# Kernel optimization log

Measured on AMD Instinct MI355X. Metric: run time of the kernel, lower is better.

Reference implementation:

```python
import jax, jax.numpy as jnp
import numpy as np

N_NODES = 50000
N_EDGES = 800000
IN_CH = 64
HID = 64
E_FEAT = 16


def _gcn_conv(x, W, b, row, col, n_nodes):
    """PyG-style GCNConv: add self loops, symmetric normalization,
    aggregate messages from source (row) at target (col)."""
    h = x @ W  # [N, H]
    loops = jnp.arange(n_nodes, dtype=row.dtype)
    r = jnp.concatenate([row, loops])
    c = jnp.concatenate([col, loops])
    ones = jnp.ones(r.shape[0], dtype=h.dtype)
    deg = jax.ops.segment_sum(ones, c, num_segments=n_nodes)  # in-degree incl. self loop
    dinv = jnp.where(deg > 0, deg ** -0.5, 0.0)
    norm = dinv[r] * dinv[c]  # [E+N]
    msg = h[r] * norm[:, None]  # gather + scale
    out = jax.ops.segment_sum(msg, c, num_segments=n_nodes)  # scatter-add at targets
    return out + b


def setup_inputs() -> dict:
    key = jax.random.key(0)
    ks = jax.random.split(key, 10)
    x = jax.random.normal(ks[0], (N_NODES, IN_CH), dtype=jnp.float32)
    eIndex = jax.random.randint(ks[1], (2, N_EDGES), 0, N_NODES, dtype=jnp.int32)
    eAttributes = jax.random.normal(ks[2], (N_EDGES, E_FEAT), dtype=jnp.float32)
    s1 = 1.0 / np.sqrt(IN_CH)
    s2 = 1.0 / np.sqrt(HID)
    sm = 1.0 / np.sqrt(2 * HID + E_FEAT)
    W1 = jax.random.uniform(ks[3], (IN_CH, HID), jnp.float32, -s1, s1)
    b1 = jnp.zeros((HID,), jnp.float32)
    W2 = jax.random.uniform(ks[4], (HID, HID), jnp.float32, -s2, s2)
    b2 = jnp.zeros((HID,), jnp.float32)
    mW1 = jax.random.uniform(ks[5], (2 * HID + E_FEAT, HID), jnp.float32, -sm, sm)
    mb1 = jax.random.uniform(ks[6], (HID,), jnp.float32, -sm, sm)
    mW2 = jax.random.uniform(ks[7], (HID, 1), jnp.float32, -s2, s2)
    mb2 = jax.random.uniform(ks[8], (1,), jnp.float32, -s2, s2)
    return {"x": x, "eIndex": eIndex, "eAttributes": eAttributes,
            "W1": W1, "b1": b1, "W2": W2, "b2": b2,
            "mW1": mW1, "mb1": mb1, "mW2": mW2, "mb2": mb2}


def reference(x, eIndex, eAttributes, W1, b1, W2, b2, mW1, mb1, mW2, mb2):
    row, col = eIndex[0], eIndex[1]
    n = x.shape[0]
    h = _gcn_conv(x, W1, b1, row, col, n)
    h = jax.nn.relu(h)
    h = _gcn_conv(h, W2, b2, row, col, n)
    # edge gather-concat-MLP
    ef = jnp.concatenate([h[row], h[col], eAttributes], axis=1)  # [E, 2H+F]
    out = jax.nn.relu(ef @ mW1 + mb1) @ mW2 + mb2  # [E, 1]
    return out
```

## Files before the change

### kernel.cpp

```cpp
#include <hip/hip_runtime.h>
#include <hip/hip_bf16.h>
#include <hip/hip_fp16.h>

#define N_NODES 50000
#define N_EDGES 800000
#define E_FEAT 16
#define BUCKET 64
#define NSL 200
#define SLW 250
#define P1B 200
#define EPB 4000
#define QCAP 64
#define GEMM1_BLOCKS 512

typedef _Float16 half4_t __attribute__((ext_vector_type(4)));
typedef _Float16 half8_t __attribute__((ext_vector_type(8)));
typedef float f32x4 __attribute__((ext_vector_type(4)));

template <int NF, bool DUAL, bool SCALE>
__device__ __forceinline__ void gemm_body(const float* __restrict__ X,
                                          const float* __restrict__ WA,
                                          const float* __restrict__ WB,
                                          const float* __restrict__ scale,
                                          const float* __restrict__ bias,
                                          __half* __restrict__ YA, __half* __restrict__ YB,
                                          int N, int wid, int nw, int lane) {
    int grp = lane >> 4, sub = lane & 15;

    half4_t wf[NF][4];
#pragma unroll
    for (int fc = 0; fc < NF; ++fc) {
        const float* Wsrc = (DUAL && fc >= NF / 2) ? WB : WA;
        int f = 16 * (DUAL ? (fc % (NF / 2)) : fc) + sub;
#pragma unroll
        for (int kc = 0; kc < 4; ++kc)
#pragma unroll
            for (int i = 0; i < 4; ++i)
                wf[fc][kc][i] = (_Float16)Wsrc[(16 * kc + 4 * grp + i) * 64 + f];
    }
    float bval[NF];
#pragma unroll
    for (int fc = 0; fc < NF; ++fc)
        bval[fc] = (DUAL && fc < NF / 2) ? bias[16 * fc + sub] : 0.0f;

    int ntiles = N >> 4;
    for (int t = wid; t < ntiles; t += nw) {
        int r0 = t << 4;
        half4_t a[4];
#pragma unroll
        for (int kc = 0; kc < 4; ++kc) {
            float4 xv = *(const float4*)(X + (size_t)(r0 + sub) * 64 + 16 * kc + 4 * grp);
            a[kc][0] = (_Float16)xv.x; a[kc][1] = (_Float16)xv.y;
            a[kc][2] = (_Float16)xv.z; a[kc][3] = (_Float16)xv.w;
        }
        f32x4 acc[NF];
#pragma unroll
        for (int fc = 0; fc < NF; ++fc) {
            float b = bval[fc];
            acc[fc][0] = b; acc[fc][1] = b; acc[fc][2] = b; acc[fc][3] = b;
        }
#pragma unroll
        for (int fc = 0; fc < NF; ++fc)
#pragma unroll
            for (int kc = 0; kc < 4; ++kc)
                acc[fc] = __builtin_amdgcn_mfma_f32_16x16x16f16(a[kc], wf[fc][kc], acc[fc], 0, 0, 0);

        float scv[4] = {1.f, 1.f, 1.f, 1.f};
        if (SCALE) {
            float4 sc = *(const float4*)(scale + r0 + 4 * grp);
            scv[0] = sc.x; scv[1] = sc.y; scv[2] = sc.z; scv[3] = sc.w;
        }
#pragma unroll
        for (int fc = 0; fc < NF; ++fc) {
            __half* Y = (DUAL && fc >= NF / 2) ? YB : YA;
            int f = 16 * (DUAL ? (fc % (NF / 2)) : fc) + sub;
#pragma unroll
            for (int reg = 0; reg < 4; ++reg) {
                float v = acc[fc][reg];
                if (SCALE) v *= scv[reg];
                Y[(size_t)(r0 + 4 * grp + reg) * 64 + f] = __float2half_rn(v);
            }
        }
    }
}

template <int NF, bool DUAL, bool SCALE>
__global__ void gemm_mfma_kernel(const float* __restrict__ X,
                                 const float* __restrict__ WA, const float* __restrict__ WB,
                                 const float* __restrict__ scale, const float* __restrict__ bias,
                                 __half* __restrict__ YA, __half* __restrict__ YB, int N) {
    int lane = threadIdx.x & 63;
    int wid = (blockIdx.x * blockDim.x + threadIdx.x) >> 6;
    int nw = (gridDim.x * blockDim.x) >> 6;
    gemm_body<NF, DUAL, SCALE>(X, WA, WB, scale, bias, YA, YB, N, wid, nw, lane);
}

__global__ void partition_gemm_kernel(const int* __restrict__ row, const int* __restrict__ col,
                                      unsigned int* __restrict__ queue, int* __restrict__ lens,
                                      const float* __restrict__ X, const float* __restrict__ W,
                                      __half* __restrict__ Y, int N) {
    if (blockIdx.x < P1B) {
        __shared__ int cur[NSL];
        for (int i = threadIdx.x; i < NSL; i += blockDim.x) cur[i] = 0;
        __syncthreads();
        int b = blockIdx.x;
        int base = b * EPB;
        for (int e = base + (int)threadIdx.x * 4; e < base + EPB; e += blockDim.x * 4) {
            int4 c4 = *(const int4*)(col + e);
            int4 r4 = *(const int4*)(row + e);
            int s, p;
            s = c4.x / SLW; p = atomicAdd(&cur[s], 1);
            if (p < QCAP) queue[(size_t)(b * NSL + s) * QCAP + p] = ((unsigned)c4.x << 16) | (unsigned)r4.x;
            s = c4.y / SLW; p = atomicAdd(&cur[s], 1);
            if (p < QCAP) queue[(size_t)(b * NSL + s) * QCAP + p] = ((unsigned)c4.y << 16) | (unsigned)r4.y;
            s = c4.z / SLW; p = atomicAdd(&cur[s], 1);
            if (p < QCAP) queue[(size_t)(b * NSL + s) * QCAP + p] = ((unsigned)c4.z << 16) | (unsigned)r4.z;
            s = c4.w / SLW; p = atomicAdd(&cur[s], 1);
            if (p < QCAP) queue[(size_t)(b * NSL + s) * QCAP + p] = ((unsigned)c4.w << 16) | (unsigned)r4.w;
        }
        __syncthreads();
        for (int i = threadIdx.x; i < NSL; i += blockDim.x)
            lens[b * NSL + i] = min(cur[i], QCAP);
    } else {
        int lane = threadIdx.x & 63;
        int wid = ((blockIdx.x - P1B) * 256 + (int)threadIdx.x) >> 6;
        int nw = (GEMM1_BLOCKS * 256) >> 6;
        gemm_body<4, false, false>(X, W, W, nullptr, nullptr, Y, Y, N, wid, nw, lane);
    }
}

__global__ void scatter3_kernel(const unsigned int* __restrict__ queue,
                                const int* __restrict__ lens,
                                int* __restrict__ cnt, float* __restrict__ dinv,
                                unsigned short* __restrict__ srcIdx) {
    __shared__ int lcnt[SLW];
    int s = blockIdx.x;
    for (int i = threadIdx.x; i < SLW; i += blockDim.x) lcnt[i] = 0;
    __syncthreads();
    int cbase = s * SLW;
    if (threadIdx.x < P1B) {
        int b = threadIdx.x;
        int len = lens[b * NSL + s];
        const unsigned int* q = queue + (size_t)(b * NSL + s) * QCAP;
        unsigned int nxt = (len > 0) ? q[0] : 0u;
        for (int i = 0; i < len; ++i) {
            unsigned int pr = nxt;
            if (i + 1 < len) nxt = q[i + 1];
            int c = (int)(pr >> 16);
            int r = (int)(pr & 0xffffu);
            int p = atomicAdd(&lcnt[c - cbase], 1);
            if (p < BUCKET) srcIdx[(c << 6) + p] = (unsigned short)r;
        }
    }
    __syncthreads();
    for (int i = threadIdx.x; i < SLW; i += blockDim.x) {
        int d = lcnt[i];
        cnt[cbase + i] = d;
        dinv[cbase + i] = rsqrtf((float)d + 1.0f);
    }
}

template <bool RELU, bool SRCSCALED>
__global__ void agg_bucket_kernel(const float2* __restrict__ hs4,
                                  const int* __restrict__ cnt,
                                  const float* __restrict__ dinv,
                                  const unsigned short* __restrict__ srcIdx,
                                  const float* __restrict__ b,
                                  float4* __restrict__ out, int N) {
    int lane = threadIdx.x & 63;
    int n = blockIdx.x * (blockDim.x >> 6) + (threadIdx.x >> 6);
    if (n >= N) return;
    int g = lane >> 4;
    int sub = lane & 15;
    int o = n << 6;
    int d = min(cnt[n], BUCKET);
    float dinvn = dinv[n];
    float4 acc = make_float4(0.f, 0.f, 0.f, 0.f);
    if (g == 0) {
        float2 raw = hs4[(size_t)n * 16 + sub];
        float2 a01 = __half22float2(*(const __half2*)&raw.x);
        float2 a23 = __half22float2(*(const __half2*)&raw.y);
        float w = SRCSCALED ? 1.0f : dinvn;
        acc.x = a01.x * w; acc.y = a01.y * w;
        acc.z = a23.x * w; acc.w = a23.y * w;
    }
    int j = g;
    for (; j + 12 < d; j += 16) {
        int s0 = srcIdx[o + j],     s1 = srcIdx[o + j + 4];
        int s2 = srcIdx[o + j + 8], s3 = srcIdx[o + j + 12];
        float2 v0 = hs4[(size_t)s0 * 16 + sub];
        float2 v1 = hs4[(size_t)s1 * 16 + sub];
        float2 v2 = hs4[(size_t)s2 * 16 + sub];
        float2 v3 = hs4[(size_t)s3 * 16 + sub];
        float w0 = 1.f, w1 = 1.f, w2 = 1.f, w3 = 1.f;
        if (!SRCSCALED) {
            w0 = rsqrtf((float)cnt[s0] + 1.f); w1 = rsqrtf((float)cnt[s1] + 1.f);
            w2 = rsqrtf((float)cnt[s2] + 1.f); w3 = rsqrtf((float)cnt[s3] + 1.f);
        }
        float2 a01 = __half22float2(*(const __half2*)&v0.x);
        float2 a23 = __half22float2(*(const __half2*)&v0.y);
        float2 b01 = __half22float2(*(const __half2*)&v1.x);
        float2 b23 = __half22float2(*(const __half2*)&v1.y);
        float2 c01 = __half22float2(*(const __half2*)&v2.x);
        float2 c23 = __half22float2(*(const __half2*)&v2.y);
        float2 d01 = __half22float2(*(const __half2*)&v3.x);
        float2 d23 = __half22float2(*(const __half2*)&v3.y);
        acc.x = fmaf(a01.x, w0, fmaf(b01.x, w1, fmaf(c01.x, w2, fmaf(d01.x, w3, acc.x))));
        acc.y = fmaf(a01.y, w0, fmaf(b01.y, w1, fmaf(c01.y, w2, fmaf(d01.y, w3, acc.y))));
        acc.z = fmaf(a23.x, w0, fmaf(b23.x, w1, fmaf(c23.x, w2, fmaf(d23.x, w3, acc.z))));
        acc.w = fmaf(a23.y, w0, fmaf(b23.y, w1, fmaf(c23.y, w2, fmaf(d23.y, w3, acc.w))));
    }
    for (; j + 4 < d; j += 8) {
        int s0 = srcIdx[o + j];
        int s1 = srcIdx[o + j + 4];
        float2 v0 = hs4[(size_t)s0 * 16 + sub];
        float2 v1 = hs4[(size_t)s1 * 16 + sub];
        float w0 = 1.f, w1 = 1.f;
        if (!SRCSCALED) {
            w0 = rsqrtf((float)cnt[s0] + 1.f); w1 = rsqrtf((float)cnt[s1] + 1.f);
        }
        float2 a01 = __half22float2(*(const __half2*)&v0.x);
        float2 a23 = __half22float2(*(const __half2*)&v0.y);
        float2 b01 = __half22float2(*(const __half2*)&v1.x);
        float2 b23 = __half22float2(*(const __half2*)&v1.y);
        acc.x = fmaf(a01.x, w0, fmaf(b01.x, w1, acc.x));
        acc.y = fmaf(a01.y, w0, fmaf(b01.y, w1, acc.y));
        acc.z = fmaf(a23.x, w0, fmaf(b23.x, w1, acc.z));
        acc.w = fmaf(a23.y, w0, fmaf(b23.y, w1, acc.w));
    }
    for (; j < d; j += 4) {
        int s0 = srcIdx[o + j];
        float2 v = hs4[(size_t)s0 * 16 + sub];
        float w0 = SRCSCALED ? 1.f : rsqrtf((float)cnt[s0] + 1.f);
        float2 a01 = __half22float2(*(const __half2*)&v.x);
        float2 a23 = __half22float2(*(const __half2*)&v.y);
        acc.x = fmaf(a01.x, w0, acc.x); acc.y = fmaf(a01.y, w0, acc.y);
        acc.z = fmaf(a23.x, w0, acc.z); acc.w = fmaf(a23.y, w0, acc.w);
    }
    acc.x += __shfl_xor(acc.x, 16); acc.y += __shfl_xor(acc.y, 16);
    acc.z += __shfl_xor(acc.z, 16); acc.w += __shfl_xor(acc.w, 16);
    acc.x += __shfl_xor(acc.x, 32); acc.y += __shfl_xor(acc.y, 32);
    acc.z += __shfl_xor(acc.z, 32); acc.w += __shfl_xor(acc.w, 32);
    if (g == 0) {
        float4 bb = ((const float4*)b)[sub];
        float4 v;
        v.x = fmaf(dinvn, acc.x, bb.x); v.y = fmaf(dinvn, acc.y, bb.y);
        v.z = fmaf(dinvn, acc.z, bb.z); v.w = fmaf(dinvn, acc.w, bb.w);
        if (RELU) {
            v.x = fmaxf(v.x, 0.f); v.y = fmaxf(v.y, 0.f);
            v.z = fmaxf(v.z, 0.f); v.w = fmaxf(v.w, 0.f);
        }
        out[(size_t)n * 16 + sub] = v;
    }
}

__global__ void edge_mlp6_kernel(const __half* __restrict__ P16, const __half* __restrict__ Q16,
                                 const int* __restrict__ row, const int* __restrict__ col,
                                 const float* __restrict__ eAtt,
                                 const float* __restrict__ mW1,
                                 const float* __restrict__ mW2, const float* __restrict__ mb2,
                                 float* __restrict__ out, int E) {
    int lane = threadIdx.x & 63;
    int grp = lane >> 4;
    int sub = lane & 15;

    half4_t aC0, aC1, aC2, aC3;
#pragma unroll
    for (int i = 0; i < 4; ++i) {
        const float* crow = mW1 + (size_t)(128 + 4 * grp + i) * 64 + 4 * sub;
        aC0[i] = (_Float16)crow[0];
        aC1[i] = (_Float16)crow[1];
        aC2[i] = (_Float16)crow[2];
        aC3[i] = (_Float16)crow[3];
    }
    float4 w20 = ((const float4*)mW2)[4 * grp + 0];
    float4 w21 = ((const float4*)mW2)[4 * grp + 1];
    float4 w22 = ((const float4*)mW2)[4 * grp + 2];
    float4 w23 = ((const float4*)mW2)[4 * grp + 3];
    float b2v = mb2[0];

    int wid = (blockIdx.x * blockDim.x + threadIdx.x) >> 6;
    int nw = (gridDim.x * blockDim.x) >> 6;
    const int ntiles = E >> 4;

    int rA = 0, cA = 0, rB = 0, cB = 0;
    if (wid < ntiles) {
        rA = __builtin_nontemporal_load(row + (wid << 4) + sub);
        cA = __builtin_nontemporal_load(col + (wid << 4) + sub);
    }
    if (wid + nw < ntiles) {
        rB = __builtin_nontemporal_load(row + ((wid + nw) << 4) + sub);
        cB = __builtin_nontemporal_load(col + ((wid + nw) << 4) + sub);
    }

    int t = wid;
    for (; t + nw < ntiles; t += 2 * nw) {
        int eA0 = t << 4, eB0 = (t + nw) << 4;

        f32x4 efA = __builtin_nontemporal_load((const f32x4*)(eAtt + (size_t)eA0 * 16) + (size_t)sub * 4 + grp);
        f32x4 efB = __builtin_nontemporal_load((const f32x4*)(eAtt + (size_t)eB0 * 16) + (size_t)sub * 4 + grp);
        const half8_t* prA = (const half8_t*)(P16 + (size_t)rA * 64 + grp * 16);
        const half8_t* qrA = (const half8_t*)(Q16 + (size_t)cA * 64 + grp * 16);
        const half8_t* prB = (const half8_t*)(P16 + (size_t)rB * 64 + grp * 16);
        const half8_t* qrB = (const half8_t*)(Q16 + (size_t)cB * 64 + grp * 16);
        half8_t phA0 = prA[0], phA1 = prA[1], qhA0 = qrA[0], qhA1 = qrA[1];
        half8_t phB0 = prB[0], phB1 = prB[1], qhB0 = qrB[0], qhB1 = qrB[1];

        int tn1 = t + 2 * nw, tn2 = t + 3 * nw;
        int rA2 = 0, cA2 = 0, rB2 = 0, cB2 = 0;
        if (tn1 < ntiles) {
            rA2 = __builtin_nontemporal_load(row + (tn1 << 4) + sub);
            cA2 = __builtin_nontemporal_load(col + (tn1 << 4) + sub);
        }
        if (tn2 < ntiles) {
            rB2 = __builtin_nontemporal_load(row + (tn2 << 4) + sub);
            cB2 = __builtin_nontemporal_load(col + (tn2 << 4) + sub);
        }

        half4_t bfA;
        bfA[0] = (_Float16)efA[0]; bfA[1] = (_Float16)efA[1];
        bfA[2] = (_Float16)efA[2]; bfA[3] = (_Float16)efA[3];
        f32x4 cin0 = {(float)phA0[0] + (float)qhA0[0], (float)phA0[4] + (float)qhA0[4],
                      (float)phA1[0] + (float)qhA1[0], (float)phA1[4] + (float)qhA1[4]};
        f32x4 cin1 = {(float)phA0[1] + (float)qhA0[1], (float)phA0[5] + (float)qhA0[5],
                      (float)phA1[1] + (float)qhA1[1], (float)phA1[5] + (float)qhA1[5]};
        f32x4 cin2 = {(float)phA0[2] + (float)qhA0[2], (float)phA0[6] + (float)qhA0[6],
                      (float)phA1[2] + (float)qhA1[2], (float)phA1[6] + (float)qhA1[6]};
        f32x4 cin3 = {(float)phA0[3] + (float)qhA0[3], (float)phA0[7] + (float)qhA0[7],
                      (float)phA1[3] + (float)qhA1[3], (float)phA1[7] + (float)qhA1[7]};
        f32x4 d0 = __builtin_amdgcn_mfma_f32_16x16x16f16(aC0, bfA, cin0, 0, 0, 0);
        f32x4 d1 = __builtin_amdgcn_mfma_f32_16x16x16f16(aC1, bfA, cin1, 0, 0, 0);
        f32x4 d2 = __builtin_amdgcn_mfma_f32_16x16x16f16(aC2, bfA, cin2, 0, 0, 0);
        f32x4 d3 = __builtin_amdgcn_mfma_f32_16x16x16f16(aC3, bfA, cin3, 0, 0, 0);
        float taccA = fmaxf(d0[0], 0.f) * w20.x + fmaxf(d0[1], 0.f) * w21.x
                    + fmaxf(d0[2], 0.f) * w22.x + fmaxf(d0[3], 0.f) * w23.x;
        taccA += fmaxf(d1[0], 0.f) * w20.y + fmaxf(d1[1], 0.f) * w21.y
               + fmaxf(d1[2], 0.f) * w22.y + fmaxf(d1[3], 0.f) * w23.y;
        taccA += fmaxf(d2[0], 0.f) * w20.z + fmaxf(d2[1], 0.f) * w21.z
               + fmaxf(d2[2], 0.f) * w22.z + fmaxf(d2[3], 0.f) * w23.z;
        taccA += fmaxf(d3[0], 0.f) * w20.w + fmaxf(d3[1], 0.f) * w21.w
               + fmaxf(d3[2], 0.f) * w22.w + fmaxf(d3[3], 0.f) * w23.w;

        half4_t bfB;
        bfB[0] = (_Float16)efB[0]; bfB[1] = (_Float16)efB[1];
        bfB[2] = (_Float16)efB[2]; bfB[3] = (_Float16)efB[3];
        cin0 = f32x4{(float)phB0[0] + (float)qhB0[0], (float)phB0[4] + (float)qhB0[4],
                     (float)phB1[0] + (float)qhB1[0], (float)phB1[4] + (float)qhB1[4]};
        cin1 = f32x4{(float)phB0[1] + (float)qhB0[1], (float)phB0[5] + (float)qhB0[5],
                     (float)phB1[1] + (float)qhB1[1], (float)phB1[5] + (float)qhB1[5]};
        cin2 = f32x4{(float)phB0[2] + (float)qhB0[2], (float)phB0[6] + (float)qhB0[6],
                     (float)phB1[2] + (float)qhB1[2], (float)phB1[6] + (float)qhB1[6]};
        cin3 = f32x4{(float)phB0[3] + (float)qhB0[3], (float)phB0[7] + (float)qhB0[7],
                     (float)phB1[3] + (float)qhB1[3], (float)phB1[7] + (float)qhB1[7]};
        d0 = __builtin_amdgcn_mfma_f32_16x16x16f16(aC0, bfB, cin0, 0, 0, 0);
        d1 = __builtin_amdgcn_mfma_f32_16x16x16f16(aC1, bfB, cin1, 0, 0, 0);
        d2 = __builtin_amdgcn_mfma_f32_16x16x16f16(aC2, bfB, cin2, 0, 0, 0);
        d3 = __builtin_amdgcn_mfma_f32_16x16x16f16(aC3, bfB, cin3, 0, 0, 0);
        float taccB = fmaxf(d0[0], 0.f) * w20.x + fmaxf(d0[1], 0.f) * w21.x
                    + fmaxf(d0[2], 0.f) * w22.x + fmaxf(d0[3], 0.f) * w23.x;
        taccB += fmaxf(d1[0], 0.f) * w20.y + fmaxf(d1[1], 0.f) * w21.y
               + fmaxf(d1[2], 0.f) * w22.y + fmaxf(d1[3], 0.f) * w23.y;
        taccB += fmaxf(d2[0], 0.f) * w20.z + fmaxf(d2[1], 0.f) * w21.z
               + fmaxf(d2[2], 0.f) * w22.z + fmaxf(d2[3], 0.f) * w23.z;
        taccB += fmaxf(d3[0], 0.f) * w20.w + fmaxf(d3[1], 0.f) * w21.w
               + fmaxf(d3[2], 0.f) * w22.w + fmaxf(d3[3], 0.f) * w23.w;

        taccA += __shfl_xor(taccA, 16); taccB += __shfl_xor(taccB, 16);
        taccA += __shfl_xor(taccA, 32); taccB += __shfl_xor(taccB, 32);
        if (grp == 0) {
            __builtin_nontemporal_store(taccA + b2v, out + eA0 + sub);
            __builtin_nontemporal_store(taccB + b2v, out + eB0 + sub);
        }

        rA = rA2; cA = cA2; rB = rB2; cB = cB2;
    }
    if (t < ntiles) {
        int e0 = t << 4;
        f32x4 ef = __builtin_nontemporal_load((const f32x4*)(eAtt + (size_t)e0 * 16) + (size_t)sub * 4 + grp);
        half4_t bf;
        bf[0] = (_Float16)ef[0]; bf[1] = (_Float16)ef[1];
        bf[2] = (_Float16)ef[2]; bf[3] = (_Float16)ef[3];
        const half8_t* pr = (const half8_t*)(P16 + (size_t)rA * 64 + grp * 16);
        const half8_t* qr = (const half8_t*)(Q16 + (size_t)cA * 64 + grp * 16);
        half8_t ph0 = pr[0], ph1 = pr[1], qh0 = qr[0], qh1 = qr[1];
        f32x4 cin0 = {(float)ph0[0] + (float)qh0[0], (float)ph0[4] + (float)qh0[4],
                      (float)ph1[0] + (float)qh1[0], (float)ph1[4] + (float)qh1[4]};
        f32x4 cin1 = {(float)ph0[1] + (float)qh0[1], (float)ph0[5] + (float)qh0[5],
                      (float)ph1[1] + (float)qh1[1], (float)ph1[5] + (float)qh1[5]};
        f32x4 cin2 = {(float)ph0[2] + (float)qh0[2], (float)ph0[6] + (float)qh0[6],
                      (float)ph1[2] + (float)qh1[2], (float)ph1[6] + (float)qh1[6]};
        f32x4 cin3 = {(float)ph0[3] + (float)qh0[3], (float)ph0[7] + (float)qh0[7],
                      (float)ph1[3] + (float)qh1[3], (float)ph1[7] + (float)qh1[7]};
        f32x4 d0 = __builtin_amdgcn_mfma_f32_16x16x16f16(aC0, bf, cin0, 0, 0, 0);
        f32x4 d1 = __builtin_amdgcn_mfma_f32_16x16x16f16(aC1, bf, cin1, 0, 0, 0);
        f32x4 d2 = __builtin_amdgcn_mfma_f32_16x16x16f16(aC2, bf, cin2, 0, 0, 0);
        f32x4 d3 = __builtin_amdgcn_mfma_f32_16x16x16f16(aC3, bf, cin3, 0, 0, 0);
        float tacc = fmaxf(d0[0], 0.f) * w20.x + fmaxf(d0[1], 0.f) * w21.x
                   + fmaxf(d0[2], 0.f) * w22.x + fmaxf(d0[3], 0.f) * w23.x;
        tacc += fmaxf(d1[0], 0.f) * w20.y + fmaxf(d1[1], 0.f) * w21.y
              + fmaxf(d1[2], 0.f) * w22.y + fmaxf(d1[3], 0.f) * w23.y;
        tacc += fmaxf(d2[0], 0.f) * w20.z + fmaxf(d2[1], 0.f) * w21.z
              + fmaxf(d2[2], 0.f) * w22.z + fmaxf(d2[3], 0.f) * w23.z;
        tacc += fmaxf(d3[0], 0.f) * w20.w + fmaxf(d3[1], 0.f) * w21.w
              + fmaxf(d3[2], 0.f) * w22.w + fmaxf(d3[3], 0.f) * w23.w;
        tacc += __shfl_xor(tacc, 16);
        tacc += __shfl_xor(tacc, 32);
        if (grp == 0) __builtin_nontemporal_store(tacc + b2v, out + e0 + sub);
    }
}

extern "C" void kernel_launch(void* const* d_in, const int* in_sizes, int n_in,
                              void* d_out, int out_size, void* d_ws, size_t ws_size,
                              hipStream_t stream) {
    const float* x    = (const float*)d_in[0];
    const int*   eIdx = (const int*)d_in[1];
    const float* eAtt = (const float*)d_in[2];
    const float* W1   = (const float*)d_in[3];
    const float* b1   = (const float*)d_in[4];
    const float* W2   = (const float*)d_in[5];
    const float* b2   = (const float*)d_in[6];
    const float* mW1  = (const float*)d_in[7];
    const float* mb1  = (const float*)d_in[8];
    const float* mW2  = (const float*)d_in[9];
    const float* mb2  = (const float*)d_in[10];
    float* out = (float*)d_out;

    const int N = N_NODES;
    const int E = N_EDGES;
    const int* row = eIdx;
    const int* col = eIdx + E;

    int*            cnt    = (int*)d_ws;
    float*          dinv   = (float*)(cnt + ((N + 63) & ~63));
    int*            lens   = (int*)(dinv + ((N + 63) & ~63));
    unsigned int*   queue  = (unsigned int*)(lens + P1B * NSL);
    unsigned short* srcIdx = (unsigned short*)(queue + (size_t)P1B * NSL * QCAP);
    __half*         h16    = (__half*)(srcIdx + (size_t)N * BUCKET);
    float*          bufB   = (float*)(h16 + (size_t)2 * N * 64);
    __half*         P16    = h16;
    __half*         Q16    = h16 + (size_t)N * 64;

    const int aggBlocks = (N + 3) / 4;

    partition_gemm_kernel<<<P1B + GEMM1_BLOCKS, 256, 0, stream>>>(
        row, col, queue, lens, x, W1, h16, N);
    scatter3_kernel<<<NSL, 256, 0, stream>>>(queue, lens, cnt, dinv, srcIdx);

    agg_bucket_kernel<true, false><<<aggBlocks, 256, 0, stream>>>(
        (const float2*)h16, cnt, dinv, srcIdx, b1, (float4*)bufB, N);

    gemm_mfma_kernel<4, false, true><<<800, 256, 0, stream>>>(
        bufB, W2, W2, dinv, nullptr, h16, h16, N);
    agg_bucket_kernel<false, true><<<aggBlocks, 256, 0, stream>>>(
        (const float2*)h16, cnt, dinv, srcIdx, b2, (float4*)bufB, N);

    gemm_mfma_kernel<8, true, false><<<800, 256, 0, stream>>>(
        bufB, mW1, mW1 + 64 * 64, nullptr, mb1, P16, Q16, N);

    edge_mlp6_kernel<<<3125, 256, 0, stream>>>(
        P16, Q16, row, col, eAtt, mW1, mW2, mb2, out, E);
}
```

Before: 139.4 us.

## Fuse neighbor aggregation with following dense GEMM via LDS staging

Each aggregation kernel now processes 16 nodes per block, writes the aggregated rows into shared memory, then runs the 64x64 MFMA GEMM on that tile directly. This replaces the separate aggregation and GEMM launches for both GCN layers and drops the fp32 intermediate buffer round trip through global memory. A separate half buffer (hs2) avoids reading and writing h16 in the same kernel. The edge MLP grid is also reduced from 3125 to 2048 blocks. The tradeoff is fewer nodes in flight per block during the gather phase, plus a block-wide barrier and redundant weight loads per block.

```diff
diff --git a/kernel.cpp b/kernel.cpp
--- a/kernel.cpp
+++ b/kernel.cpp
@@ -12,36 +12,29 @@
 #define EPB 4000
 #define QCAP 64
 #define GEMM1_BLOCKS 512
+#define HSTRIDE 72
 
 typedef _Float16 half4_t __attribute__((ext_vector_type(4)));
 typedef _Float16 half8_t __attribute__((ext_vector_type(8)));
 typedef float f32x4 __attribute__((ext_vector_type(4)));
 
-template <int NF, bool DUAL, bool SCALE>
+template <int NF>
 __device__ __forceinline__ void gemm_body(const float* __restrict__ X,
-                                          const float* __restrict__ WA,
-                                          const float* __restrict__ WB,
-                                          const float* __restrict__ scale,
-                                          const float* __restrict__ bias,
-                                          __half* __restrict__ YA, __half* __restrict__ YB,
+                                          const float* __restrict__ W,
+                                          __half* __restrict__ Y,
                                           int N, int wid, int nw, int lane) {
     int grp = lane >> 4, sub = lane & 15;
 
     half4_t wf[NF][4];
 #pragma unroll
     for (int fc = 0; fc < NF; ++fc) {
-        const float* Wsrc = (DUAL && fc >= NF / 2) ? WB : WA;
-        int f = 16 * (DUAL ? (fc % (NF / 2)) : fc) + sub;
+        int f = 16 * fc + sub;
 #pragma unroll
         for (int kc = 0; kc < 4; ++kc)
 #pragma unroll
             for (int i = 0; i < 4; ++i)
-                wf[fc][kc][i] = (_Float16)Wsrc[(16 * kc + 4 * grp + i) * 64 + f];
-    }
-    float bval[NF];
-#pragma unroll
-    for (int fc = 0; fc < NF; ++fc)
-        bval[fc] = (DUAL && fc < NF / 2) ? bias[16 * fc + sub] : 0.0f;
+                wf[fc][kc][i] = (_Float16)W[(16 * kc + 4 * grp + i) * 64 + f];
+    }
 
     int ntiles = N >> 4;
     for (int t = wid; t < ntiles; t += nw) {
@@ -55,44 +48,20 @@
         }
         f32x4 acc[NF];
 #pragma unroll
-        for (int fc = 0; fc < NF; ++fc) {
-            float b = bval[fc];
-            acc[fc][0] = b; acc[fc][1] = b; acc[fc][2] = b; acc[fc][3] = b;
-        }
+        for (int fc = 0; fc < NF; ++fc) { acc[fc][0] = 0; acc[fc][1] = 0; acc[fc][2] = 0; acc[fc][3] = 0; }
 #pragma unroll
         for (int fc = 0; fc < NF; ++fc)
 #pragma unroll
             for (int kc = 0; kc < 4; ++kc)
                 acc[fc] = __builtin_amdgcn_mfma_f32_16x16x16f16(a[kc], wf[fc][kc], acc[fc], 0, 0, 0);
-
-        float scv[4] = {1.f, 1.f, 1.f, 1.f};
-        if (SCALE) {
-            float4 sc = *(const float4*)(scale + r0 + 4 * grp);
-            scv[0] = sc.x; scv[1] = sc.y; scv[2] = sc.z; scv[3] = sc.w;
-        }
 #pragma unroll
         for (int fc = 0; fc < NF; ++fc) {
-            __half* Y = (DUAL && fc >= NF / 2) ? YB : YA;
-            int f = 16 * (DUAL ? (fc % (NF / 2)) : fc) + sub;
-#pragma unroll
-            for (int reg = 0; reg < 4; ++reg) {
-                float v = acc[fc][reg];
-                if (SCALE) v *= scv[reg];
-                Y[(size_t)(r0 + 4 * grp + reg) * 64 + f] = __float2half_rn(v);
-            }
-        }
-    }
-}
-
-template <int NF, bool DUAL, bool SCALE>
-__global__ void gemm_mfma_kernel(const float* __restrict__ X,
-                                 const float* __restrict__ WA, const float* __restrict__ WB,
-                                 const float* __restrict__ scale, const float* __restrict__ bias,
-                                 __half* __restrict__ YA, __half* __restrict__ YB, int N) {
-    int lane = threadIdx.x & 63;
-    int wid = (blockIdx.x * blockDim.x + threadIdx.x) >> 6;
-    int nw = (gridDim.x * blockDim.x) >> 6;
-    gemm_body<NF, DUAL, SCALE>(X, WA, WB, scale, bias, YA, YB, N, wid, nw, lane);
+            int f = 16 * fc + sub;
+#pragma unroll
+            for (int reg = 0; reg < 4; ++reg)
+                Y[(size_t)(r0 + 4 * grp + reg) * 64 + f] = __float2half_rn(acc[fc][reg]);
+        }
+    }
 }
 
 __global__ void partition_gemm_kernel(const int* __restrict__ row, const int* __restrict__ col,
@@ -125,7 +94,7 @@
         int lane = threadIdx.x & 63;
         int wid = ((blockIdx.x - P1B) * 256 + (int)threadIdx.x) >> 6;
         int nw = (GEMM1_BLOCKS * 256) >> 6;
-        gemm_body<4, false, false>(X, W, W, nullptr, nullptr, Y, Y, N, wid, nw, lane);
+        gemm_body<4>(X, W, Y, N, wid, nw, lane);
     }
 }
 
@@ -160,97 +129,146 @@
     }
 }
 
-template <bool RELU, bool SRCSCALED>
-__global__ void agg_bucket_kernel(const float2* __restrict__ hs4,
-                                  const int* __restrict__ cnt,
-                                  const float* __restrict__ dinv,
-                                  const unsigned short* __restrict__ srcIdx,
-                                  const float* __restrict__ b,
-                                  float4* __restrict__ out, int N) {
+template <bool RELU_H, bool SRCSCALED, bool DUALOUT, bool SCALEOUT>
+__global__ void fused_agg_gemm_kernel(const float2* __restrict__ hs4,
+                                      const int* __restrict__ cnt,
+                                      const float* __restrict__ dinv,
+                                      const unsigned short* __restrict__ srcIdx,
+                                      const float* __restrict__ bagg,
+                                      const float* __restrict__ WA, const float* __restrict__ WB,
+                                      const float* __restrict__ biasP,
+                                      __half* __restrict__ YA, __half* __restrict__ YB, int N) {
+    __shared__ float hlds[16 * HSTRIDE];
     int lane = threadIdx.x & 63;
-    int n = blockIdx.x * (blockDim.x >> 6) + (threadIdx.x >> 6);
-    if (n >= N) return;
+    int w = threadIdx.x >> 6;
     int g = lane >> 4;
     int sub = lane & 15;
-    int o = n << 6;
-    int d = min(cnt[n], BUCKET);
-    float dinvn = dinv[n];
-    float4 acc = make_float4(0.f, 0.f, 0.f, 0.f);
-    if (g == 0) {
-        float2 raw = hs4[(size_t)n * 16 + sub];
-        float2 a01 = __half22float2(*(const __half2*)&raw.x);
-        float2 a23 = __half22float2(*(const __half2*)&raw.y);
-        float w = SRCSCALED ? 1.0f : dinvn;
-        acc.x = a01.x * w; acc.y = a01.y * w;
-        acc.z = a23.x * w; acc.w = a23.y * w;
-    }
-    int j = g;
-    for (; j + 12 < d; j += 16) {
-        int s0 = srcIdx[o + j],     s1 = srcIdx[o + j + 4];
-        int s2 = srcIdx[o + j + 8], s3 = srcIdx[o + j + 12];
-        float2 v0 = hs4[(size_t)s0 * 16 + sub];
-        float2 v1 = hs4[(size_t)s1 * 16 + sub];
-        float2 v2 = hs4[(size_t)s2 * 16 + sub];
-        float2 v3 = hs4[(size_t)s3 * 16 + sub];
-        float w0 = 1.f, w1 = 1.f, w2 = 1.f, w3 = 1.f;
-        if (!SRCSCALED) {
-            w0 = rsqrtf((float)cnt[s0] + 1.f); w1 = rsqrtf((float)cnt[s1] + 1.f);
-            w2 = rsqrtf((float)cnt[s2] + 1.f); w3 = rsqrtf((float)cnt[s3] + 1.f);
-        }
-        float2 a01 = __half22float2(*(const __half2*)&v0.x);
-        float2 a23 = __half22float2(*(const __half2*)&v0.y);
-        float2 b01 = __half22float2(*(const __half2*)&v1.x);
-        float2 b23 = __half22float2(*(const __half2*)&v1.y);
-        float2 c01 = __half22float2(*(const __half2*)&v2.x);
-        float2 c23 = __half22float2(*(const __half2*)&v2.y);
-        float2 d01 = __half22float2(*(const __half2*)&v3.x);
-        float2 d23 = __half22float2(*(const __half2*)&v3.y);
-        acc.x = fmaf(a01.x, w0, fmaf(b01.x, w1, fmaf(c01.x, w2, fmaf(d01.x, w3, acc.x))));
-        acc.y = fmaf(a01.y, w0, fmaf(b01.y, w1, fmaf(c01.y, w2, fmaf(d01.y, w3, acc.y))));
-        acc.z = fmaf(a23.x, w0, fmaf(b23.x, w1, fmaf(c23.x, w2, fmaf(d23.x, w3, acc.z))));
-        acc.w = fmaf(a23.y, w0, fmaf(b23.y, w1, fmaf(c23.y, w2, fmaf(d23.y, w3, acc.w))));
-    }
-    for (; j + 4 < d; j += 8) {
-        int s0 = srcIdx[o + j];
-        int s1 = srcIdx[o + j + 4];
-        float2 v0 = hs4[(size_t)s0 * 16 + sub];
-        float2 v1 = hs4[(size_t)s1 * 16 + sub];
-        float w0 = 1.f, w1 = 1.f;
-        if (!SRCSCALED) {
-            w0 = rsqrtf((float)cnt[s0] + 1.f); w1 = rsqrtf((float)cnt[s1] + 1.f);
-        }
-        float2 a01 = __half22float2(*(const __half2*)&v0.x);
-        float2 a23 = __half22float2(*(const __half2*)&v0.y);
-        float2 b01 = __half22float2(*(const __half2*)&v1.x);
-        float2 b23 = __half22float2(*(const __half2*)&v1.y);
-        acc.x = fmaf(a01.x, w0, fmaf(b01.x, w1, acc.x));
-        acc.y = fmaf(a01.y, w0, fmaf(b01.y, w1, acc.y));
-        acc.z = fmaf(a23.x, w0, fmaf(b23.x, w1, acc.z));
-        acc.w = fmaf(a23.y, w0, fmaf(b23.y, w1, acc.w));
-    }
-    for (; j < d; j += 4) {
-        int s0 = srcIdx[o + j];
-        float2 v = hs4[(size_t)s0 * 16 + sub];
-        float w0 = SRCSCALED ? 1.f : rsqrtf((float)cnt[s0] + 1.f);
-        float2 a01 = __half22float2(*(const __half2*)&v.x);
-        float2 a23 = __half22float2(*(const __half2*)&v.y);
-        acc.x = fmaf(a01.x, w0, acc.x); acc.y = fmaf(a01.y, w0, acc.y);
-        acc.z = fmaf(a23.x, w0, acc.z); acc.w = fmaf(a23.y, w0, acc.w);
-    }
-    acc.x += __shfl_xor(acc.x, 16); acc.y += __shfl_xor(acc.y, 16);
-    acc.z += __shfl_xor(acc.z, 16); acc.w += __shfl_xor(acc.w, 16);
-    acc.x += __shfl_xor(acc.x, 32); acc.y += __shfl_xor(acc.y, 32);
-    acc.z += __shfl_xor(acc.z, 32); acc.w += __shfl_xor(acc.w, 32);
-    if (g == 0) {
-        float4 bb = ((const float4*)b)[sub];
-        float4 v;
-        v.x = fmaf(dinvn, acc.x, bb.x); v.y = fmaf(dinvn, acc.y, bb.y);
-        v.z = fmaf(dinvn, acc.z, bb.z); v.w = fmaf(dinvn, acc.w, bb.w);
-        if (RELU) {
-            v.x = fmaxf(v.x, 0.f); v.y = fmaxf(v.y, 0.f);
-            v.z = fmaxf(v.z, 0.f); v.w = fmaxf(v.w, 0.f);
-        }
-        out[(size_t)n * 16 + sub] = v;
+    int grp = g;
+    int n0 = blockIdx.x << 4;
+
+    for (int k = 0; k < 4; ++k) {
+        int n = n0 + 4 * w + k;
+        int o = n << 6;
+        int d = min(cnt[n], BUCKET);
+        float dinvn = dinv[n];
+        float4 acc = make_float4(0.f, 0.f, 0.f, 0.f);
+        if (g == 0) {
+            float2 raw = hs4[(size_t)n * 16 + sub];
+            float2 a01 = __half22float2(*(const __half2*)&raw.x);
+            float2 a23 = __half22float2(*(const __half2*)&raw.y);
+            float ws = SRCSCALED ? 1.0f : dinvn;
+            acc.x = a01.x * ws; acc.y = a01.y * ws;
+            acc.z = a23.x * ws; acc.w = a23.y * ws;
+        }
+        int j = g;
+        for (; j + 12 < d; j += 16) {
+            int s0 = srcIdx[o + j],     s1 = srcIdx[o + j + 4];
+            int s2 = srcIdx[o + j + 8], s3 = srcIdx[o + j + 12];
+            float2 v0 = hs4[(size_t)s0 * 16 + sub];
+            float2 v1 = hs4[(size_t)s1 * 16 + sub];
+            float2 v2 = hs4[(size_t)s2 * 16 + sub];
+            float2 v3 = hs4[(size_t)s3 * 16 + sub];
+            float w0 = 1.f, w1 = 1.f, w2 = 1.f, w3 = 1.f;
+            if (!SRCSCALED) {
+                w0 = rsqrtf((float)cnt[s0] + 1.f); w1 = rsqrtf((float)cnt[s1] + 1.f);
+                w2 = rsqrtf((float)cnt[s2] + 1.f); w3 = rsqrtf((float)cnt[s3] + 1.f);
+            }
+            float2 a01 = __half22float2(*(const __half2*)&v0.x);
+            float2 a23 = __half22float2(*(const __half2*)&v0.y);
+            float2 b01 = __half22float2(*(const __half2*)&v1.x);
+            float2 b23 = __half22float2(*(const __half2*)&v1.y);
+            float2 c01 = __half22float2(*(const __half2*)&v2.x);
+            float2 c23 = __half22float2(*(const __half2*)&v2.y);
+            float2 d01 = __half22float2(*(const __half2*)&v3.x);
+            float2 d23 = __half22float2(*(const __half2*)&v3.y);
+            acc.x = fmaf(a01.x, w0, fmaf(b01.x, w1, fmaf(c01.x, w2, fmaf(d01.x, w3, acc.x))));
+            acc.y = fmaf(a01.y, w0, fmaf(b01.y, w1, fmaf(c01.y, w2, fmaf(d01.y, w3, acc.y))));
+            acc.z = fmaf(a23.x, w0, fmaf(b23.x, w1, fmaf(c23.x, w2, fmaf(d23.x, w3, acc.z))));
+            acc.w = fmaf(a23.y, w0, fmaf(b23.y, w1, fmaf(c23.y, w2, fmaf(d23.y, w3, acc.w))));
+        }
+        for (; j + 4 < d; j += 8) {
+            int s0 = srcIdx[o + j];
+            int s1 = srcIdx[o + j + 4];
+            float2 v0 = hs4[(size_t)s0 * 16 + sub];
+            float2 v1 = hs4[(size_t)s1 * 16 + sub];
+            float w0 = 1.f, w1 = 1.f;
+            if (!SRCSCALED) {
+                w0 = rsqrtf((float)cnt[s0] + 1.f); w1 = rsqrtf((float)cnt[s1] + 1.f);
+            }
+            float2 a01 = __half22float2(*(const __half2*)&v0.x);
+            float2 a23 = __half22float2(*(const __half2*)&v0.y);
+            float2 b01 = __half22float2(*(const __half2*)&v1.x);
+            float2 b23 = __half22float2(*(const __half2*)&v1.y);
+            acc.x = fmaf(a01.x, w0, fmaf(b01.x, w1, acc.x));
+            acc.y = fmaf(a01.y, w0, fmaf(b01.y, w1, acc.y));
+            acc.z = fmaf(a23.x, w0, fmaf(b23.x, w1, acc.z));
+            acc.w = fmaf(a23.y, w0, fmaf(b23.y, w1, acc.w));
+        }
+        for (; j < d; j += 4) {
+            int s0 = srcIdx[o + j];
+            float2 v = hs4[(size_t)s0 * 16 + sub];
+            float w0 = SRCSCALED ? 1.f : rsqrtf((float)cnt[s0] + 1.f);
+            float2 a01 = __half22float2(*(const __half2*)&v.x);
+            float2 a23 = __half22float2(*(const __half2*)&v.y);
+            acc.x = fmaf(a01.x, w0, acc.x); acc.y = fmaf(a01.y, w0, acc.y);
+            acc.z = fmaf(a23.x, w0, acc.z); acc.w = fmaf(a23.y, w0, acc.w);
+        }
+        acc.x += __shfl_xor(acc.x, 16); acc.y += __shfl_xor(acc.y, 16);
+        acc.z += __shfl_xor(acc.z, 16); acc.w += __shfl_xor(acc.w, 16);
+        acc.x += __shfl_xor(acc.x, 32); acc.y += __shfl_xor(acc.y, 32);
+        acc.z += __shfl_xor(acc.z, 32); acc.w += __shfl_xor(acc.w, 32);
+        if (g == 0) {
+            float4 bb = ((const float4*)bagg)[sub];
+            float4 v;
+            v.x = fmaf(dinvn, acc.x, bb.x); v.y = fmaf(dinvn, acc.y, bb.y);
+            v.z = fmaf(dinvn, acc.z, bb.z); v.w = fmaf(dinvn, acc.w, bb.w);
+            if (RELU_H) {
+                v.x = fmaxf(v.x, 0.f); v.y = fmaxf(v.y, 0.f);
+                v.z = fmaxf(v.z, 0.f); v.w = fmaxf(v.w, 0.f);
+            }
+            *(float4*)&hlds[(4 * w + k) * HSTRIDE + 4 * sub] = v;
+        }
+    }
+    __syncthreads();
+
+    int f = 16 * w + sub;
+    half4_t wfa[4], wfb[4];
+#pragma unroll
+    for (int kc = 0; kc < 4; ++kc)
+#pragma unroll
+        for (int i = 0; i < 4; ++i) {
+            wfa[kc][i] = (_Float16)WA[(16 * kc + 4 * grp + i) * 64 + f];
+            if (DUALOUT) wfb[kc][i] = (_Float16)WB[(16 * kc + 4 * grp + i) * 64 + f];
+        }
+
+    half4_t a[4];
+#pragma unroll
+    for (int kc = 0; kc < 4; ++kc) {
+        float4 xv = *(const float4*)&hlds[sub * HSTRIDE + 16 * kc + 4 * grp];
+        a[kc][0] = (_Float16)xv.x; a[kc][1] = (_Float16)xv.y;
+        a[kc][2] = (_Float16)xv.z; a[kc][3] = (_Float16)xv.w;
+    }
+
+    float bp = DUALOUT ? biasP[f] : 0.0f;
+    f32x4 accA = {bp, bp, bp, bp};
+    f32x4 accB = {0.f, 0.f, 0.f, 0.f};
+#pragma unroll
+    for (int kc = 0; kc < 4; ++kc) {
+        accA = __builtin_amdgcn_mfma_f32_16x16x16f16(a[kc], wfa[kc], accA, 0, 0, 0);
+        if (DUALOUT) accB = __builtin_amdgcn_mfma_f32_16x16x16f16(a[kc], wfb[kc], accB, 0, 0, 0);
+    }
+
+    float scv[4] = {1.f, 1.f, 1.f, 1.f};
+    if (SCALEOUT) {
+        float4 sc = *(const float4*)(dinv + n0 + 4 * grp);
+        scv[0] = sc.x; scv[1] = sc.y; scv[2] = sc.z; scv[3] = sc.w;
+    }
+#pragma unroll
+    for (int reg = 0; reg < 4; ++reg) {
+        float vA = accA[reg];
+        if (SCALEOUT) vA *= scv[reg];
+        YA[(size_t)(n0 + 4 * grp + reg) * 64 + f] = __float2half_rn(vA);
+        if (DUALOUT) YB[(size_t)(n0 + 4 * grp + reg) * 64 + f] = __float2half_rn(accB[reg]);
     }
 }
 
@@ -436,27 +454,24 @@
     unsigned int*   queue  = (unsigned int*)(lens + P1B * NSL);
     unsigned short* srcIdx = (unsigned short*)(queue + (size_t)P1B * NSL * QCAP);
     __half*         h16    = (__half*)(srcIdx + (size_t)N * BUCKET);
-    float*          bufB   = (float*)(h16 + (size_t)2 * N * 64);
     __half*         P16    = h16;
     __half*         Q16    = h16 + (size_t)N * 64;
-
-    const int aggBlocks = (N + 3) / 4;
+    __half*         hs2    = (__half*)(h16 + (size_t)2 * N * 64);
+
+    const int fusedBlocks = N / 16;
 
     partition_gemm_kernel<<<P1B + GEMM1_BLOCKS, 256, 0, stream>>>(
         row, col, queue, lens, x, W1, h16, N);
     scatter3_kernel<<<NSL, 256, 0, stream>>>(queue, lens, cnt, dinv, srcIdx);
 
-    agg_bucket_kernel<true, false><<<aggBlocks, 256, 0, stream>>>(
-        (const float2*)h16, cnt, dinv, srcIdx, b1, (float4*)bufB, N);
-
-    gemm_mfma_kernel<4, false, true><<<800, 256, 0, stream>>>(
-        bufB, W2, W2, dinv, nullptr, h16, h16, N);
-    agg_bucket_kernel<false, true><<<aggBlocks, 256, 0, stream>>>(
-        (const float2*)h16, cnt, dinv, srcIdx, b2, (float4*)bufB, N);
-
-    gemm_mfma_kernel<8, true, false><<<800, 256, 0, stream>>>(
-        bufB, mW1, mW1 + 64 * 64, nullptr, mb1, P16, Q16, N);
-
-    edge_mlp6_kernel<<<3125, 256, 0, stream>>>(
+    fused_agg_gemm_kernel<true, false, false, true><<<fusedBlocks, 256, 0, stream>>>(
+        (const float2*)h16, cnt, dinv, srcIdx, b1,
+        W2, W2, nullptr, hs2, hs2, N);
+
+    fused_agg_gemm_kernel<false, true, true, false><<<fusedBlocks, 256, 0, stream>>>(
+        (const float2*)hs2, cnt, dinv, srcIdx, b2,
+        mW1, mW1 + 64 * 64, mb1, P16, Q16, N);
+
+    edge_mlp6_kernel<<<2048, 256, 0, stream>>>(
         P16, Q16, row, col, eAtt, mW1, mW2, mb2, out, E);
 }
```

Result: faster. 120.7 us (-13.4%).
